# Performance work log

Hardware: AMD Instinct MI355X
Metric: run time of the kernel (lower is better)

Reference implementation:

```python
import jax, jax.numpy as jnp
import numpy as np

DIM = 1024
HEADS = 16
DIM_HEAD = 64
INNER = HEADS * DIM_HEAD
LN_EPS = 1e-5


def setup_inputs() -> dict:
    key = jax.random.key(0)
    ks = jax.random.split(key, 7)
    b, n = 2, 2048
    x = jax.random.normal(ks[0], (b, n, DIM), dtype=jnp.float32)
    attn_bias = jax.random.normal(ks[1], (HEADS, n, n), dtype=jnp.float32)
    gamma = jnp.ones((DIM,), dtype=jnp.float32)
    beta = jnp.zeros((DIM,), dtype=jnp.float32)
    wq = jax.random.normal(ks[2], (DIM, INNER), dtype=jnp.float32) * (DIM ** -0.5)
    wkv = jax.random.normal(ks[3], (DIM, 2 * INNER), dtype=jnp.float32) * (DIM ** -0.5)
    wo = jax.random.normal(ks[4], (INNER, DIM), dtype=jnp.float32) * (INNER ** -0.5)
    return {"x": x, "attn_bias": attn_bias, "gamma": gamma, "beta": beta,
            "wq": wq, "wkv": wkv, "wo": wo}


def reference(x, attn_bias, gamma, beta, wq, wkv, wo):
    b, n, _ = x.shape
    scale = DIM_HEAD ** -0.5
    # LayerNorm
    mu = jnp.mean(x, axis=-1, keepdims=True)
    var = jnp.var(x, axis=-1, keepdims=True)
    xn = (x - mu) * jax.lax.rsqrt(var + LN_EPS) * gamma + beta
    # QKV projections
    q = xn @ wq                      # [b, n, inner]
    kv = xn @ wkv                    # [b, n, 2*inner]
    k, v = jnp.split(kv, 2, axis=-1)
    split_heads = lambda t: t.reshape(b, n, HEADS, DIM_HEAD).transpose(0, 2, 1, 3)
    q, k, v = map(split_heads, (q, k, v))  # [b, h, n, d]
    q = q * scale
    sim = jnp.einsum('bhid,bhjd->bhij', q, k)
    sim = sim + attn_bias[None]      # broadcast over batch
    causal_mask = jnp.triu(jnp.ones((n, n), dtype=bool), k=1)
    sim = jnp.where(causal_mask, -jnp.finfo(sim.dtype).max, sim)
    attn = jax.nn.softmax(sim, axis=-1)
    out = jnp.einsum('bhij,bhjd->bhid', attn, v)
    out = out.transpose(0, 2, 1, 3).reshape(b, n, INNER)
    return out @ wo
```

## Files before the change

### kernel.cpp

```cpp
#include <hip/hip_runtime.h>
#include <hip/hip_bf16.h>

#define DIM   1024
#define HEADS 16
#define DHEAD 64
#define INNER 1024
#define NSEQ  2048
#define NB    2
#define MROWS (NB * NSEQ)
#define QS    (3 * INNER)

typedef __attribute__((ext_vector_type(8))) short    short8;
typedef __attribute__((ext_vector_type(4))) short    short4v;
typedef __attribute__((ext_vector_type(4))) float    floatx4;
typedef __attribute__((ext_vector_type(8))) _Float16 half8;

#define GLOBAL_AS __attribute__((address_space(1)))
#define LDS_AS    __attribute__((address_space(3)))

static __device__ __forceinline__ short f2h(float f) {
  _Float16 h = (_Float16)f;
  return __builtin_bit_cast(short, h);
}
static __device__ __forceinline__ float h2f(short s) {
  return (float)__builtin_bit_cast(_Float16, s);
}

static __device__ __forceinline__ floatx4 mfma16(short8 a, short8 b, floatx4 c) {
  return __builtin_amdgcn_mfma_f32_16x16x32_f16(
      __builtin_bit_cast(half8, a), __builtin_bit_cast(half8, b), c, 0, 0, 0);
}

__device__ __constant__ signed char kQtTab[40] = {
  15,14,13,12,11,10,9,8,7,6,5,4,3,
  15,14,13,12,11,10,9,8,7,
  15,14,13,12,11,
  15,
  2,6,10,14,
  1,5,9,13,
  0,4,8,12};
__device__ __constant__ signed char kCTab[40] = {
  0,0,0,0,0,0,0,0,0,0,0,0,0,
  1,1,1,1,1,1,1,1,1,
  2,2,2,2,2,
  3,
  0,1,2,3,
  0,1,2,3,
  0,1,2,3};
__device__ __constant__ signed char kSlotTab[16][4] = {
  {36,-1,-1,-1},{32,-1,-1,-1},{28,-1,-1,-1},{12,-1,-1,-1},
  {11,37,-1,-1},{10,33,-1,-1},{ 9,29,-1,-1},{ 8,21,-1,-1},
  { 7,20,38,-1},{ 6,19,34,-1},{ 5,18,30,-1},{ 4,17,26,-1},
  { 3,16,25,39},{ 2,15,24,35},{ 1,14,23,31},{ 0,13,22,27}};

__global__ __launch_bounds__(256) void ln_kernel(const float* __restrict__ x,
                                                 const float* __restrict__ gamma,
                                                 const float* __restrict__ beta,
                                                 short* __restrict__ xn) {
  int row = blockIdx.x;
  int t   = threadIdx.x;
  const float4* xr = reinterpret_cast<const float4*>(x + (size_t)row * DIM);
  float4 v = xr[t];
  float s  = v.x + v.y + v.z + v.w;
  float s2 = v.x * v.x + v.y * v.y + v.z * v.z + v.w * v.w;
#pragma unroll
  for (int off = 1; off < 64; off <<= 1) {
    s  += __shfl_xor(s, off);
    s2 += __shfl_xor(s2, off);
  }
  __shared__ float red[8];
  if ((t & 63) == 0) { red[t >> 6] = s; red[(t >> 6) + 4] = s2; }
  __syncthreads();
  s  = red[0] + red[1] + red[2] + red[3];
  s2 = red[4] + red[5] + red[6] + red[7];
  float mu   = s * (1.0f / DIM);
  float var  = s2 * (1.0f / DIM) - mu * mu;
  float rstd = rsqrtf(var + 1e-5f);
  float4 g  = reinterpret_cast<const float4*>(gamma)[t];
  float4 bb = reinterpret_cast<const float4*>(beta)[t];
  short4v o;
  o.x = f2h((v.x - mu) * rstd * g.x + bb.x);
  o.y = f2h((v.y - mu) * rstd * g.y + bb.y);
  o.z = f2h((v.z - mu) * rstd * g.z + bb.z);
  o.w = f2h((v.w - mu) * rstd * g.w + bb.w);
  reinterpret_cast<short4v*>(xn + (size_t)row * DIM)[t] = o;
}

__global__ __launch_bounds__(256) void transpose_f16(const float* __restrict__ w,
                                                     short* __restrict__ wt,
                                                     int Kk, int Nn) {
  __shared__ float tile[32][33];
  int n0 = blockIdx.x * 32, k0 = blockIdx.y * 32;
  int tx = threadIdx.x & 31, ty = threadIdx.x >> 5;
#pragma unroll
  for (int i = 0; i < 32; i += 8)
    tile[ty + i][tx] = w[(size_t)(k0 + ty + i) * Nn + n0 + tx];
  __syncthreads();
#pragma unroll
  for (int i = 0; i < 32; i += 8)
    wt[(size_t)(n0 + ty + i) * Kk + k0 + tx] = f2h(tile[tx][ty + i]);
}

template <bool F32OUT>
__global__ __launch_bounds__(256) void gemm_bt(const short* __restrict__ A,
                                               const short* __restrict__ Bt,
                                               void* __restrict__ Cout,
                                               int Nn, int Kk,
                                               float oscale, float oscale2,
                                               int qsplit) {
  constexpr int BM = 128, BN = 128, BK = 64;
  __shared__ __attribute__((aligned(16))) short As[BM * BK];
  __shared__ __attribute__((aligned(16))) short Bs[BN * BK];
  int bm = blockIdx.x, bn = blockIdx.y;
  int t = threadIdx.x, lane = t & 63, w = t >> 6;
  int l15 = lane & 15, lhi = lane >> 4;
  int wr = w >> 1, wc = w & 1;
  float osc = (bn * BN < qsplit) ? oscale : oscale2;
  floatx4 acc[4][4] = {};
  const short* Ag = A + (size_t)bm * BM * Kk;
  const short* Bg = Bt + (size_t)bn * BN * Kk;

  for (int k0 = 0; k0 < Kk; k0 += BK) {
#pragma unroll
    for (int it = 0; it < 4; ++it) {
      int base = it * 256 + w * 64;
      int idx  = base + lane;
      int row  = idx >> 3, kc = (idx & 7) << 3;
      __builtin_amdgcn_global_load_lds(
          (const GLOBAL_AS unsigned int*)(Ag + (size_t)row * Kk + k0 + kc),
          (LDS_AS unsigned int*)(As + base * 8), 16, 0, 0);
    }
#pragma unroll
    for (int it = 0; it < 4; ++it) {
      int base = it * 256 + w * 64;
      int idx  = base + lane;
      int row  = idx >> 3, kc = (idx & 7) << 3;
      __builtin_amdgcn_global_load_lds(
          (const GLOBAL_AS unsigned int*)(Bg + (size_t)row * Kk + k0 + kc),
          (LDS_AS unsigned int*)(Bs + base * 8), 16, 0, 0);
    }
    __syncthreads();
#pragma unroll
    for (int kc = 0; kc < 2; ++kc) {
      short8 a[4], b[4];
#pragma unroll
      for (int mt = 0; mt < 4; ++mt)
        a[mt] = *reinterpret_cast<const short8*>(
            &As[(wr * 64 + mt * 16 + l15) * BK + lhi * 8 + kc * 32]);
#pragma unroll
      for (int nt = 0; nt < 4; ++nt)
        b[nt] = *reinterpret_cast<const short8*>(
            &Bs[(wc * 64 + nt * 16 + l15) * BK + lhi * 8 + kc * 32]);
#pragma unroll
      for (int mt = 0; mt < 4; ++mt)
#pragma unroll
        for (int nt = 0; nt < 4; ++nt)
          acc[mt][nt] = mfma16(a[mt], b[nt], acc[mt][nt]);
    }
    __syncthreads();
  }

  int row0 = bm * BM + wr * 64;
  int col0 = bn * BN + wc * 64;
#pragma unroll
  for (int mt = 0; mt < 4; ++mt)
#pragma unroll
    for (int nt = 0; nt < 4; ++nt)
#pragma unroll
      for (int r = 0; r < 4; ++r) {
        int row = row0 + mt * 16 + lhi * 4 + r;
        int col = col0 + nt * 16 + l15;
        if (F32OUT)
          ((float*)Cout)[(size_t)row * Nn + col] = acc[mt][nt][r] * osc;
        else
          ((short*)Cout)[(size_t)row * Nn + col] = f2h(acc[mt][nt][r] * osc);
      }
}

__global__ __launch_bounds__(512) void attn_kernel(const short* __restrict__ qkv,
                                                   const float* __restrict__ bias,
                                                   short* __restrict__ ao,
                                                   short* __restrict__ Opart,
                                                   float* __restrict__ mlpart) {
  __shared__ __attribute__((aligned(16))) short Ks[2][2][4096];
  __shared__ __attribute__((aligned(16))) short Vt[2][4096];
  __shared__ __attribute__((aligned(16))) short Ps[128 * 72];

  int p = blockIdx.x;
  int rank = p >> 4, h = p & 15;
  int qt = kQtTab[rank], c = kCTab[rank];
  int tt0 = c * 8;
  int tt1 = 2 * qt + 2; if (tt0 + 8 < tt1) tt1 = tt0 + 8;
  int qb = qt * 128;
  int t = threadIdx.x, lane = t & 63, w = t >> 6;
  int l15 = lane & 15, lhi = lane >> 4;

  short8 qf[2][2];
#pragma unroll
  for (int bb = 0; bb < 2; ++bb) {
    const short* qrow = qkv +
        ((size_t)(bb * NSEQ + qb + w * 16 + l15)) * QS + h * DHEAD + lhi * 8;
    qf[bb][0] = *reinterpret_cast<const short8*>(qrow);
    qf[bb][1] = *reinterpret_cast<const short8*>(qrow + 32);
  }

  int krow = t >> 3;
  int kcg  = (t & 7) ^ (krow & 7);
  int vrr = (t >> 4) * 2, vcc = (t & 15) << 2;
  short4v vr[2][2];

  auto issueK = [&](int tile, int nb) {
#pragma unroll
    for (int bb = 0; bb < 2; ++bb) {
      const short* gp = qkv +
          ((size_t)(bb * NSEQ + tile * 64 + krow)) * QS + INNER + h * DHEAD + kcg * 8;
      __builtin_amdgcn_global_load_lds(
          (const GLOBAL_AS unsigned int*)gp,
          (LDS_AS unsigned int*)(&Ks[nb][bb][0] + (size_t)w * 512), 16, 0, 0);
    }
  };
  auto issueV = [&](int tile) {
#pragma unroll
    for (int bb = 0; bb < 2; ++bb) {
      const short* vp = qkv + ((size_t)(bb * NSEQ + tile * 64 + vrr)) * QS +
                        2 * INNER + h * DHEAD + vcc;
      vr[bb][0] = *reinterpret_cast<const short4v*>(vp);
      vr[bb][1] = *reinterpret_cast<const short4v*>(vp + QS);
    }
  };
  auto writeV = [&]() {
#pragma unroll
    for (int bb = 0; bb < 2; ++bb)
#pragma unroll
      for (int e = 0; e < 4; ++e) {
        int d  = vcc + e;
        int jj = vrr ^ ((d & 7) << 3);
        unsigned int pk = (unsigned short)vr[bb][0][e] |
                          ((unsigned int)(unsigned short)vr[bb][1][e] << 16);
        *reinterpret_cast<unsigned int*>(&Vt[bb][d * 64 + jj]) = pk;
      }
  };
  auto issueB = [&](int tile, floatx4 (&br)[4]) {
    const float* bb0 = bias +
        ((size_t)h * NSEQ + (qb + w * 16 + l15)) * NSEQ + tile * 64 + lhi * 4;
#pragma unroll
    for (int jt = 0; jt < 4; ++jt)
      br[jt] = *reinterpret_cast<const floatx4*>(bb0 + jt * 16);
  };

  float m[2], l[2];
  floatx4 oacc[2][4] = {};
#pragma unroll
  for (int bb = 0; bb < 2; ++bb) { m[bb] = -1e30f; l[bb] = 0.f; }

  int swz = (l15 & 7) << 3;

  auto step = [&](int tt, int KB, floatx4 (&brU)[4], floatx4 (&brN)[4]) {
    bool more = (tt + 1 < tt1);
    if (more) { issueK(tt + 1, KB ^ 1); issueV(tt + 1); issueB(tt + 1, brN); }

#pragma unroll
    for (int bb = 0; bb < 2; ++bb) {
      floatx4 s[4];
#pragma unroll
      for (int jt = 0; jt < 4; ++jt) s[jt] = brU[jt];

#pragma unroll
      for (int jt = 0; jt < 4; ++jt) {
        int ro = (jt * 16 + l15) * 64;
        short8 k0 = *reinterpret_cast<const short8*>(
            &Ks[KB][bb][ro + ((lhi * 8) ^ swz)]);
        short8 k1 = *reinterpret_cast<const short8*>(
            &Ks[KB][bb][ro + ((lhi * 8 + 32) ^ swz)]);
        s[jt] = mfma16(k0, qf[bb][0], s[jt]);
        s[jt] = mfma16(k1, qf[bb][1], s[jt]);
      }

      if (tt >= 2 * qt) {
        int dq = qb + w * 16 + l15 - tt * 64;
#pragma unroll
        for (int jt = 0; jt < 4; ++jt)
#pragma unroll
          for (int r = 0; r < 4; ++r)
            if (jt * 16 + lhi * 4 + r > dq) s[jt][r] = -1e30f;
      }

      float mx = s[0][0];
#pragma unroll
      for (int jt = 0; jt < 4; ++jt)
#pragma unroll
        for (int r = 0; r < 4; ++r) mx = fmaxf(mx, s[jt][r]);
      mx = fmaxf(mx, __shfl_xor(mx, 16));
      mx = fmaxf(mx, __shfl_xor(mx, 32));
      float mnew = fmaxf(m[bb], mx);
      float fac  = __expf(m[bb] - mnew);
      m[bb] = mnew;
      float ps = 0.f;
#pragma unroll
      for (int jt = 0; jt < 4; ++jt)
#pragma unroll
        for (int r = 0; r < 4; ++r) {
          float pv = __expf(s[jt][r] - mnew);
          s[jt][r] = pv;
          ps += pv;
        }
      ps += __shfl_xor(ps, 16);
      ps += __shfl_xor(ps, 32);
      l[bb] = l[bb] * fac + ps;

      float facr[4];
#pragma unroll
      for (int r = 0; r < 4; ++r)
        facr[r] = __shfl(fac, (lane & 48) | (lhi * 4 + r));
#pragma unroll
      for (int dt = 0; dt < 4; ++dt)
#pragma unroll
        for (int r = 0; r < 4; ++r) oacc[bb][dt][r] *= facr[r];

#pragma unroll
      for (int jt = 0; jt < 4; ++jt) {
        short4v pv4;
        pv4.x = f2h(s[jt][0]); pv4.y = f2h(s[jt][1]);
        pv4.z = f2h(s[jt][2]); pv4.w = f2h(s[jt][3]);
        *reinterpret_cast<short4v*>(
            &Ps[(w * 16 + l15) * 72 + jt * 16 + lhi * 4]) = pv4;
      }

#pragma unroll
      for (int jc = 0; jc < 2; ++jc) {
        short8 pf = *reinterpret_cast<const short8*>(
            &Ps[(w * 16 + l15) * 72 + lhi * 8 + jc * 32]);
#pragma unroll
        for (int dt = 0; dt < 4; ++dt) {
          int dd = dt * 16 + l15;
          short8 vf = *reinterpret_cast<const short8*>(
              &Vt[bb][dd * 64 + ((lhi * 8 + jc * 32) ^ swz)]);
          oacc[bb][dt] = mfma16(pf, vf, oacc[bb][dt]);
        }
      }
    }

    if (more) {
      __syncthreads();
      writeV();
      __syncthreads();
    }
  };

  floatx4 brA[4], brB[4];
  issueK(tt0, 0);
  issueV(tt0);
  issueB(tt0, brA);
  __syncthreads();
  writeV();
  __syncthreads();

  int nt = tt1 - tt0;
  for (int i = 0; i < nt; i += 2) {
    step(tt0 + i, 0, brA, brB);
    step(tt0 + i + 1, 1, brB, brA);
  }

  bool single = (tt0 == 0) && (tt1 == 2 * qt + 2);
  if (single) {
#pragma unroll
    for (int bb = 0; bb < 2; ++bb) {
      float linv = 1.f / l[bb];
      float lr[4];
#pragma unroll
      for (int r = 0; r < 4; ++r)
        lr[r] = __shfl(linv, (lane & 48) | (lhi * 4 + r));
#pragma unroll
      for (int dt = 0; dt < 4; ++dt)
#pragma unroll
        for (int r = 0; r < 4; ++r) {
          int row = qb + w * 16 + lhi * 4 + r;
          int col = h * DHEAD + dt * 16 + l15;
          ao[((size_t)(bb * NSEQ + row)) * INNER + col] =
              f2h(oacc[bb][dt][r] * lr[r]);
        }
    }
  } else {
#pragma unroll
    for (int bb = 0; bb < 2; ++bb) {
      size_t pp = ((size_t)h * 40 + rank) * 2 + bb;
      short* Ob = Opart + pp * 8192;
#pragma unroll
      for (int dt = 0; dt < 4; ++dt)
#pragma unroll
        for (int r = 0; r < 4; ++r)
          Ob[(w * 16 + lhi * 4 + r) * 64 + dt * 16 + l15] = f2h(oacc[bb][dt][r]);
      if (lhi == 0) {
        mlpart[pp * 256 + w * 16 + l15] = m[bb];
        mlpart[pp * 256 + 128 + w * 16 + l15] = l[bb];
      }
    }
  }
}

__global__ __launch_bounds__(512) void attn_combine(const short* __restrict__ Opart,
                                                    const float* __restrict__ mlpart,
                                                    short* __restrict__ o) {
  int qt = blockIdx.x + 4, h = blockIdx.y, b = blockIdx.z;
  int nc = (2 * qt + 9) >> 3;
  int t = threadIdx.x, row = t >> 2, cg = (t & 3) << 4;

  float mv[4], lv[4];
  float M = -1e30f;
#pragma unroll
  for (int c2 = 0; c2 < 4; ++c2) {
    if (c2 < nc) {
      size_t pp = ((size_t)h * 40 + kSlotTab[qt][c2]) * 2 + b;
      mv[c2] = mlpart[pp * 256 + row];
      lv[c2] = mlpart[pp * 256 + 128 + row];
      M = fmaxf(M, mv[c2]);
    }
  }

  float acc[16] = {};
  float lsum = 0.f;
#pragma unroll
  for (int c2 = 0; c2 < 4; ++c2) {
    if (c2 >= nc) break;
    float wgt = __expf(mv[c2] - M);
    lsum += wgt * lv[c2];
    size_t pp = ((size_t)h * 40 + kSlotTab[qt][c2]) * 2 + b;
    const short8* Or =
        reinterpret_cast<const short8*>(Opart + pp * 8192 + row * 64 + cg);
    short8 a0 = Or[0], a1 = Or[1];
#pragma unroll
    for (int e = 0; e < 8; ++e) {
      acc[e]     += wgt * h2f(a0[e]);
      acc[8 + e] += wgt * h2f(a1[e]);
    }
  }
  float inv = 1.f / lsum;
  short* op = o + ((size_t)(b * NSEQ + qt * 128 + row)) * INNER + h * DHEAD + cg;
  short8 o0, o1;
#pragma unroll
  for (int e = 0; e < 8; ++e) {
    o0[e] = f2h(acc[e] * inv);
    o1[e] = f2h(acc[8 + e] * inv);
  }
  reinterpret_cast<short8*>(op)[0] = o0;
  reinterpret_cast<short8*>(op)[1] = o1;
}

extern "C" void kernel_launch(void* const* d_in, const int* in_sizes, int n_in,
                              void* d_out, int out_size, void* d_ws, size_t ws_size,
                              hipStream_t stream) {
  const float* x     = (const float*)d_in[0];
  const float* bias  = (const float*)d_in[1];
  const float* gamma = (const float*)d_in[2];
  const float* beta  = (const float*)d_in[3];
  const float* wq    = (const float*)d_in[4];
  const float* wkv   = (const float*)d_in[5];
  const float* wo    = (const float*)d_in[6];
  float* out = (float*)d_out;

  char* ws = (char*)d_ws;
  const size_t MB = 1024 * 1024;
  short* xn      = (short*)(ws);
  short* wqkv_t  = (short*)(ws + 8  * MB);
  short* wo_t    = (short*)(ws + 14 * MB);
  short* qkv     = (short*)(ws + 16 * MB);
  short* Opart   = (short*)(ws + 40 * MB);
  float* mlpart  = (float*)(ws + 62 * MB);
  short* ao      = xn;

  ln_kernel<<<MROWS, 256, 0, stream>>>(x, gamma, beta, xn);
  transpose_f16<<<dim3(INNER / 32, DIM / 32), 256, 0, stream>>>(wq, wqkv_t, DIM, INNER);
  transpose_f16<<<dim3(2 * INNER / 32, DIM / 32), 256, 0, stream>>>(
      wkv, wqkv_t + (size_t)1024 * 1024, DIM, 2 * INNER);
  transpose_f16<<<dim3(DIM / 32, INNER / 32), 256, 0, stream>>>(wo, wo_t, INNER, DIM);

  gemm_bt<false><<<dim3(MROWS / 128, QS / 128), 256, 0, stream>>>(
      xn, wqkv_t, qkv, QS, DIM, 0.125f, 1.0f, 1024);

  attn_kernel<<<640, 512, 0, stream>>>(qkv, bias, ao, Opart, mlpart);
  attn_combine<<<dim3(12, HEADS, NB), 512, 0, stream>>>(Opart, mlpart, ao);

  gemm_bt<true><<<dim3(MROWS / 128, DIM / 128), 256, 0, stream>>>(
      ao, wo_t, out, DIM, INNER, 1.0f, 1.0f, 0);
}
```

Measured before the change: 172.5 us.

## Use 256x256 double-buffered tile for QKV GEMM and XCD-aware block remapping

```diff
diff --git a/kernel.cpp b/kernel.cpp
--- a/kernel.cpp
+++ b/kernel.cpp
@@ -29,6 +29,12 @@
 static __device__ __forceinline__ floatx4 mfma16(short8 a, short8 b, floatx4 c) {
   return __builtin_amdgcn_mfma_f32_16x16x32_f16(
       __builtin_bit_cast(half8, a), __builtin_bit_cast(half8, b), c, 0, 0, 0);
+}
+
+static __device__ __forceinline__ int xcd_work(int bid, int nwg) {
+  int q = nwg >> 3, r = nwg & 7;
+  int xcd = bid & 7, pos = bid >> 3;
+  return (xcd < r ? xcd * (q + 1) : r * (q + 1) + (xcd - r) * q) + pos;
 }
 
 __device__ __constant__ signed char kQtTab[40] = {
@@ -101,21 +107,104 @@
     wt[(size_t)(n0 + ty + i) * Kk + k0 + tx] = f2h(tile[tx][ty + i]);
 }
 
+__global__ __launch_bounds__(512) void gemm_bt256(const short* __restrict__ A,
+                                                  const short* __restrict__ Bt,
+                                                  short* __restrict__ Cout,
+                                                  int Nn, int Kk, int NBN,
+                                                  float oscale, float oscale2,
+                                                  int qsplit) {
+  __shared__ __attribute__((aligned(16))) short As[2][256 * 64];
+  __shared__ __attribute__((aligned(16))) short Bs[2][256 * 64];
+
+  int wk = xcd_work(blockIdx.x, gridDim.x);
+  int bm = wk / NBN, bn = wk % NBN;
+  int t = threadIdx.x, lane = t & 63, w = t >> 6;
+  int l15 = lane & 15, lhi = lane >> 4;
+  int wr = w >> 2, wc = w & 3;
+
+  const short* Ag = A + (size_t)bm * 256 * Kk;
+  const short* Bg = Bt + (size_t)bn * 256 * Kk;
+
+  auto stage = [&](int kt, int buf) {
+#pragma unroll
+    for (int it = 0; it < 4; ++it) {
+      int base = it * 512 + w * 64;
+      int g = base + lane;
+      int row = g >> 3, c8 = (g & 7) << 3;
+      __builtin_amdgcn_global_load_lds(
+          (const GLOBAL_AS unsigned int*)(Ag + (size_t)row * Kk + kt * 64 + c8),
+          (LDS_AS unsigned int*)(&As[buf][base * 8]), 16, 0, 0);
+    }
+#pragma unroll
+    for (int it = 0; it < 4; ++it) {
+      int base = it * 512 + w * 64;
+      int g = base + lane;
+      int row = g >> 3, c8 = (g & 7) << 3;
+      __builtin_amdgcn_global_load_lds(
+          (const GLOBAL_AS unsigned int*)(Bg + (size_t)row * Kk + kt * 64 + c8),
+          (LDS_AS unsigned int*)(&Bs[buf][base * 8]), 16, 0, 0);
+    }
+  };
+
+  floatx4 acc[8][4] = {};
+  int NK = Kk >> 6;
+
+  stage(0, 0);
+  __syncthreads();
+  int cur = 0;
+  for (int kt = 0; kt < NK; ++kt) {
+    if (kt + 1 < NK) stage(kt + 1, cur ^ 1);
+#pragma unroll
+    for (int kc = 0; kc < 2; ++kc) {
+      short8 a[8], b[4];
+#pragma unroll
+      for (int mt = 0; mt < 8; ++mt)
+        a[mt] = *reinterpret_cast<const short8*>(
+            &As[cur][(wr * 128 + mt * 16 + l15) * 64 + kc * 32 + lhi * 8]);
+#pragma unroll
+      for (int nt = 0; nt < 4; ++nt)
+        b[nt] = *reinterpret_cast<const short8*>(
+            &Bs[cur][(wc * 64 + nt * 16 + l15) * 64 + kc * 32 + lhi * 8]);
+#pragma unroll
+      for (int mt = 0; mt < 8; ++mt)
+#pragma unroll
+        for (int nt = 0; nt < 4; ++nt)
+          acc[mt][nt] = mfma16(a[mt], b[nt], acc[mt][nt]);
+    }
+    __syncthreads();
+    cur ^= 1;
+  }
+
+  int row0 = bm * 256 + wr * 128 + lhi * 4;
+  int col0 = bn * 256 + wc * 64 + l15;
+#pragma unroll
+  for (int mt = 0; mt < 8; ++mt)
+#pragma unroll
+    for (int nt = 0; nt < 4; ++nt) {
+      float osc = (bn * 256 + wc * 64 + nt * 16 < qsplit) ? oscale : oscale2;
+#pragma unroll
+      for (int r = 0; r < 4; ++r) {
+        int row = row0 + mt * 16 + r;
+        int col = col0 + nt * 16;
+        Cout[(size_t)row * Nn + col] = f2h(acc[mt][nt][r] * osc);
+      }
+    }
+}
+
 template <bool F32OUT>
 __global__ __launch_bounds__(256) void gemm_bt(const short* __restrict__ A,
                                                const short* __restrict__ Bt,
                                                void* __restrict__ Cout,
-                                               int Nn, int Kk,
-                                               float oscale, float oscale2,
-                                               int qsplit) {
+                                               int Nn, int Kk, int NBN,
+                                               float oscale) {
   constexpr int BM = 128, BN = 128, BK = 64;
   __shared__ __attribute__((aligned(16))) short As[BM * BK];
   __shared__ __attribute__((aligned(16))) short Bs[BN * BK];
-  int bm = blockIdx.x, bn = blockIdx.y;
+  int wk = xcd_work(blockIdx.x, gridDim.x);
+  int bm = wk / NBN, bn = wk % NBN;
   int t = threadIdx.x, lane = t & 63, w = t >> 6;
   int l15 = lane & 15, lhi = lane >> 4;
   int wr = w >> 1, wc = w & 1;
-  float osc = (bn * BN < qsplit) ? oscale : oscale2;
   floatx4 acc[4][4] = {};
   const short* Ag = A + (size_t)bm * BM * Kk;
   const short* Bg = Bt + (size_t)bn * BN * Kk;
@@ -171,9 +260,9 @@
         int row = row0 + mt * 16 + lhi * 4 + r;
         int col = col0 + nt * 16 + l15;
         if (F32OUT)
-          ((float*)Cout)[(size_t)row * Nn + col] = acc[mt][nt][r] * osc;
+          ((float*)Cout)[(size_t)row * Nn + col] = acc[mt][nt][r] * oscale;
         else
-          ((short*)Cout)[(size_t)row * Nn + col] = f2h(acc[mt][nt][r] * osc);
+          ((short*)Cout)[(size_t)row * Nn + col] = f2h(acc[mt][nt][r] * oscale);
       }
 }
 
@@ -474,12 +563,12 @@
       wkv, wqkv_t + (size_t)1024 * 1024, DIM, 2 * INNER);
   transpose_f16<<<dim3(DIM / 32, INNER / 32), 256, 0, stream>>>(wo, wo_t, INNER, DIM);
 
-  gemm_bt<false><<<dim3(MROWS / 128, QS / 128), 256, 0, stream>>>(
-      xn, wqkv_t, qkv, QS, DIM, 0.125f, 1.0f, 1024);
+  gemm_bt256<<<(MROWS / 256) * (QS / 256), 512, 0, stream>>>(
+      xn, wqkv_t, qkv, QS, DIM, QS / 256, 0.125f, 1.0f, 1024);
 
   attn_kernel<<<640, 512, 0, stream>>>(qkv, bias, ao, Opart, mlpart);
   attn_combine<<<dim3(12, HEADS, NB), 512, 0, stream>>>(Opart, mlpart, ao);
 
-  gemm_bt<true><<<dim3(MROWS / 128, DIM / 128), 256, 0, stream>>>(
-      ao, wo_t, out, DIM, INNER, 1.0f, 1.0f, 0);
-}
+  gemm_bt<true><<<(MROWS / 128) * (DIM / 128), 256, 0, stream>>>(
+      ao, wo_t, out, DIM, INNER, DIM / 128, 1.0f);
+}
```

Result: faster. 168.3 us (-2.5%).

## Double-buffer GEMM with swizzled LDS, XCD-aware tile mapping, and fuse prep kernels

Applied to the files above, without the earlier changes.

```diff
diff --git a/kernel.cpp b/kernel.cpp
--- a/kernel.cpp
+++ b/kernel.cpp
@@ -29,6 +29,12 @@
 static __device__ __forceinline__ floatx4 mfma16(short8 a, short8 b, floatx4 c) {
   return __builtin_amdgcn_mfma_f32_16x16x32_f16(
       __builtin_bit_cast(half8, a), __builtin_bit_cast(half8, b), c, 0, 0, 0);
+}
+
+static __device__ __forceinline__ int xcd_work(int bid, int nwg) {
+  int q = nwg >> 3, r = nwg & 7;
+  int xcd = bid & 7, pos = bid >> 3;
+  return (xcd < r ? xcd * (q + 1) : r * (q + 1) + (xcd - r) * q) + pos;
 }
 
 __device__ __constant__ signed char kQtTab[40] = {
@@ -53,119 +59,148 @@
   { 7,20,38,-1},{ 6,19,34,-1},{ 5,18,30,-1},{ 4,17,26,-1},
   { 3,16,25,39},{ 2,15,24,35},{ 1,14,23,31},{ 0,13,22,27}};
 
-__global__ __launch_bounds__(256) void ln_kernel(const float* __restrict__ x,
-                                                 const float* __restrict__ gamma,
-                                                 const float* __restrict__ beta,
-                                                 short* __restrict__ xn) {
-  int row = blockIdx.x;
-  int t   = threadIdx.x;
-  const float4* xr = reinterpret_cast<const float4*>(x + (size_t)row * DIM);
-  float4 v = xr[t];
-  float s  = v.x + v.y + v.z + v.w;
-  float s2 = v.x * v.x + v.y * v.y + v.z * v.z + v.w * v.w;
-#pragma unroll
-  for (int off = 1; off < 64; off <<= 1) {
-    s  += __shfl_xor(s, off);
-    s2 += __shfl_xor(s2, off);
-  }
-  __shared__ float red[8];
-  if ((t & 63) == 0) { red[t >> 6] = s; red[(t >> 6) + 4] = s2; }
+__global__ __launch_bounds__(256) void prep_kernel(
+    const float* __restrict__ x, const float* __restrict__ gamma,
+    const float* __restrict__ beta, short* __restrict__ xn,
+    const float* __restrict__ wq, const float* __restrict__ wkv,
+    const float* __restrict__ wo, short* __restrict__ wqkv_t,
+    short* __restrict__ wo_t) {
+  __shared__ float tile[32][33];
+  int bid = blockIdx.x;
+  int t = threadIdx.x;
+
+  if (bid < MROWS) {
+    const float4* xr = reinterpret_cast<const float4*>(x + (size_t)bid * DIM);
+    float4 v = xr[t];
+    float s  = v.x + v.y + v.z + v.w;
+    float s2 = v.x * v.x + v.y * v.y + v.z * v.z + v.w * v.w;
+#pragma unroll
+    for (int off = 1; off < 64; off <<= 1) {
+      s  += __shfl_xor(s, off);
+      s2 += __shfl_xor(s2, off);
+    }
+    float* red = &tile[0][0];
+    if ((t & 63) == 0) { red[t >> 6] = s; red[(t >> 6) + 4] = s2; }
+    __syncthreads();
+    s  = red[0] + red[1] + red[2] + red[3];
+    s2 = red[4] + red[5] + red[6] + red[7];
+    float mu   = s * (1.0f / DIM);
+    float var  = s2 * (1.0f / DIM) - mu * mu;
+    float rstd = rsqrtf(var + 1e-5f);
+    float4 g  = reinterpret_cast<const float4*>(gamma)[t];
+    float4 bb = reinterpret_cast<const float4*>(beta)[t];
+    short4v o;
+    o.x = f2h((v.x - mu) * rstd * g.x + bb.x);
+    o.y = f2h((v.y - mu) * rstd * g.y + bb.y);
+    o.z = f2h((v.z - mu) * rstd * g.z + bb.z);
+    o.w = f2h((v.w - mu) * rstd * g.w + bb.w);
+    reinterpret_cast<short4v*>(xn + (size_t)bid * DIM)[t] = o;
+    return;
+  }
+
+  bid -= MROWS;
+  const float* src; short* dst; int Nn, nx;
+  if (bid < 1024)      { src = wq;  dst = wqkv_t;                     Nn = 1024; nx = 32; }
+  else if (bid < 3072) { bid -= 1024; src = wkv;
+                         dst = wqkv_t + (size_t)1024 * 1024;          Nn = 2048; nx = 64; }
+  else                 { bid -= 3072; src = wo;  dst = wo_t;          Nn = 1024; nx = 32; }
+  int n0 = (bid % nx) * 32, k0 = (bid / nx) * 32;
+  int tx = t & 31, ty = t >> 5;
+#pragma unroll
+  for (int i = 0; i < 32; i += 8)
+    tile[ty + i][tx] = src[(size_t)(k0 + ty + i) * Nn + n0 + tx];
   __syncthreads();
-  s  = red[0] + red[1] + red[2] + red[3];
-  s2 = red[4] + red[5] + red[6] + red[7];
-  float mu   = s * (1.0f / DIM);
-  float var  = s2 * (1.0f / DIM) - mu * mu;
-  float rstd = rsqrtf(var + 1e-5f);
-  float4 g  = reinterpret_cast<const float4*>(gamma)[t];
-  float4 bb = reinterpret_cast<const float4*>(beta)[t];
-  short4v o;
-  o.x = f2h((v.x - mu) * rstd * g.x + bb.x);
-  o.y = f2h((v.y - mu) * rstd * g.y + bb.y);
-  o.z = f2h((v.z - mu) * rstd * g.z + bb.z);
-  o.w = f2h((v.w - mu) * rstd * g.w + bb.w);
-  reinterpret_cast<short4v*>(xn + (size_t)row * DIM)[t] = o;
-}
-
-__global__ __launch_bounds__(256) void transpose_f16(const float* __restrict__ w,
-                                                     short* __restrict__ wt,
-                                                     int Kk, int Nn) {
-  __shared__ float tile[32][33];
-  int n0 = blockIdx.x * 32, k0 = blockIdx.y * 32;
-  int tx = threadIdx.x & 31, ty = threadIdx.x >> 5;
 #pragma unroll
   for (int i = 0; i < 32; i += 8)
-    tile[ty + i][tx] = w[(size_t)(k0 + ty + i) * Nn + n0 + tx];
-  __syncthreads();
-#pragma unroll
-  for (int i = 0; i < 32; i += 8)
-    wt[(size_t)(n0 + ty + i) * Kk + k0 + tx] = f2h(tile[tx][ty + i]);
+    dst[(size_t)(n0 + ty + i) * 1024 + k0 + tx] = f2h(tile[tx][ty + i]);
 }
 
 template <bool F32OUT>
-__global__ __launch_bounds__(256) void gemm_bt(const short* __restrict__ A,
+__global__ __launch_bounds__(256) void gemm_cv(const short* __restrict__ A,
                                                const short* __restrict__ Bt,
                                                void* __restrict__ Cout,
-                                               int Nn, int Kk,
+                                               int Nn, int Kk, int NBN,
                                                float oscale, float oscale2,
                                                int qsplit) {
-  constexpr int BM = 128, BN = 128, BK = 64;
-  __shared__ __attribute__((aligned(16))) short As[BM * BK];
-  __shared__ __attribute__((aligned(16))) short Bs[BN * BK];
-  int bm = blockIdx.x, bn = blockIdx.y;
+  __shared__ __attribute__((aligned(16))) short As[2][128 * 64];
+  __shared__ __attribute__((aligned(16))) short Bs[2][128 * 64];
+  int wk = xcd_work(blockIdx.x, gridDim.x);
+  int bm = wk / NBN, bn = wk % NBN;
   int t = threadIdx.x, lane = t & 63, w = t >> 6;
   int l15 = lane & 15, lhi = lane >> 4;
   int wr = w >> 1, wc = w & 1;
-  float osc = (bn * BN < qsplit) ? oscale : oscale2;
+  const short* Ag = A + (size_t)bm * 128 * Kk;
+  const short* Bg = Bt + (size_t)bn * 128 * Kk;
+
+  auto stage = [&](int kt, int buf) {
+#pragma unroll
+    for (int it = 0; it < 4; ++it) {
+      int id = it * 256 + t;
+      int row = id >> 3;
+      int cs = ((id & 7) ^ (row & 7)) << 3;
+      __builtin_amdgcn_global_load_lds(
+          (const GLOBAL_AS unsigned int*)(Ag + (size_t)row * Kk + kt * 64 + cs),
+          (LDS_AS unsigned int*)(&As[buf][id * 8]), 16, 0, 0);
+    }
+#pragma unroll
+    for (int it = 0; it < 4; ++it) {
+      int id = it * 256 + t;
+      int row = id >> 3;
+      int cs = ((id & 7) ^ (row & 7)) << 3;
+      __builtin_amdgcn_global_load_lds(
+          (const GLOBAL_AS unsigned int*)(Bg + (size_t)row * Kk + kt * 64 + cs),
+          (LDS_AS unsigned int*)(&Bs[buf][id * 8]), 16, 0, 0);
+    }
+  };
+
   floatx4 acc[4][4] = {};
-  const short* Ag = A + (size_t)bm * BM * Kk;
-  const short* Bg = Bt + (size_t)bn * BN * Kk;
-
-  for (int k0 = 0; k0 < Kk; k0 += BK) {
-#pragma unroll
-    for (int it = 0; it < 4; ++it) {
-      int base = it * 256 + w * 64;
-      int idx  = base + lane;
-      int row  = idx >> 3, kc = (idx & 7) << 3;
-      __builtin_amdgcn_global_load_lds(
-          (const GLOBAL_AS unsigned int*)(Ag + (size_t)row * Kk + k0 + kc),
-          (LDS_AS unsigned int*)(As + base * 8), 16, 0, 0);
-    }
-#pragma unroll
-    for (int it = 0; it < 4; ++it) {
-      int base = it * 256 + w * 64;
-      int idx  = base + lane;
-      int row  = idx >> 3, kc = (idx & 7) << 3;
-      __builtin_amdgcn_global_load_lds(
-          (const GLOBAL_AS unsigned int*)(Bg + (size_t)row * Kk + k0 + kc),
-          (LDS_AS unsigned int*)(Bs + base * 8), 16, 0, 0);
-    }
-    __syncthreads();
+  int NK = Kk >> 6;
+
+  stage(0, 0);
+  stage(1, 1);
+  for (int kt = 0; kt < NK; ++kt) {
+    if (kt + 1 < NK) asm volatile("s_waitcnt vmcnt(8)" ::: "memory");
+    else             asm volatile("s_waitcnt vmcnt(0)" ::: "memory");
+    __builtin_amdgcn_s_barrier();
+    __builtin_amdgcn_sched_barrier(0);
+
+    int buf = kt & 1;
 #pragma unroll
     for (int kc = 0; kc < 2; ++kc) {
       short8 a[4], b[4];
 #pragma unroll
-      for (int mt = 0; mt < 4; ++mt)
-        a[mt] = *reinterpret_cast<const short8*>(
-            &As[(wr * 64 + mt * 16 + l15) * BK + lhi * 8 + kc * 32]);
-#pragma unroll
-      for (int nt = 0; nt < 4; ++nt)
-        b[nt] = *reinterpret_cast<const short8*>(
-            &Bs[(wc * 64 + nt * 16 + l15) * BK + lhi * 8 + kc * 32]);
+      for (int mt = 0; mt < 4; ++mt) {
+        int row = wr * 64 + mt * 16 + l15;
+        int g = (kc * 4 + lhi) ^ (l15 & 7);
+        a[mt] = *reinterpret_cast<const short8*>(&As[buf][row * 64 + g * 8]);
+      }
+#pragma unroll
+      for (int nt = 0; nt < 4; ++nt) {
+        int row = wc * 64 + nt * 16 + l15;
+        int g = (kc * 4 + lhi) ^ (l15 & 7);
+        b[nt] = *reinterpret_cast<const short8*>(&Bs[buf][row * 64 + g * 8]);
+      }
 #pragma unroll
       for (int mt = 0; mt < 4; ++mt)
 #pragma unroll
         for (int nt = 0; nt < 4; ++nt)
           acc[mt][nt] = mfma16(a[mt], b[nt], acc[mt][nt]);
     }
-    __syncthreads();
-  }
-
-  int row0 = bm * BM + wr * 64;
-  int col0 = bn * BN + wc * 64;
+
+    asm volatile("s_waitcnt lgkmcnt(0)" ::: "memory");
+    __builtin_amdgcn_sched_barrier(0);
+    __builtin_amdgcn_s_barrier();
+    __builtin_amdgcn_sched_barrier(0);
+    if (kt + 2 < NK) stage(kt + 2, buf);
+  }
+
+  int row0 = bm * 128 + wr * 64;
+  int col0 = bn * 128 + wc * 64;
 #pragma unroll
   for (int mt = 0; mt < 4; ++mt)
 #pragma unroll
-    for (int nt = 0; nt < 4; ++nt)
+    for (int nt = 0; nt < 4; ++nt) {
+      float osc = (col0 + nt * 16 < qsplit) ? oscale : oscale2;
 #pragma unroll
       for (int r = 0; r < 4; ++r) {
         int row = row0 + mt * 16 + lhi * 4 + r;
@@ -175,6 +210,7 @@
         else
           ((short*)Cout)[(size_t)row * Nn + col] = f2h(acc[mt][nt][r] * osc);
       }
+    }
 }
 
 __global__ __launch_bounds__(512) void attn_kernel(const short* __restrict__ qkv,
@@ -468,18 +504,15 @@
   float* mlpart  = (float*)(ws + 62 * MB);
   short* ao      = xn;
 
-  ln_kernel<<<MROWS, 256, 0, stream>>>(x, gamma, beta, xn);
-  transpose_f16<<<dim3(INNER / 32, DIM / 32), 256, 0, stream>>>(wq, wqkv_t, DIM, INNER);
-  transpose_f16<<<dim3(2 * INNER / 32, DIM / 32), 256, 0, stream>>>(
-      wkv, wqkv_t + (size_t)1024 * 1024, DIM, 2 * INNER);
-  transpose_f16<<<dim3(DIM / 32, INNER / 32), 256, 0, stream>>>(wo, wo_t, INNER, DIM);
-
-  gemm_bt<false><<<dim3(MROWS / 128, QS / 128), 256, 0, stream>>>(
-      xn, wqkv_t, qkv, QS, DIM, 0.125f, 1.0f, 1024);
+  prep_kernel<<<8192, 256, 0, stream>>>(x, gamma, beta, xn, wq, wkv, wo,
+                                        wqkv_t, wo_t);
+
+  gemm_cv<false><<<(MROWS / 128) * (QS / 128), 256, 0, stream>>>(
+      xn, wqkv_t, qkv, QS, DIM, QS / 128, 0.125f, 1.0f, 1024);
 
   attn_kernel<<<640, 512, 0, stream>>>(qkv, bias, ao, Opart, mlpart);
   attn_combine<<<dim3(12, HEADS, NB), 512, 0, stream>>>(Opart, mlpart, ao);
 
-  gemm_bt<true><<<dim3(MROWS / 128, DIM / 128), 256, 0, stream>>>(
-      ao, wo_t, out, DIM, INNER, 1.0f, 1.0f, 0);
-}
+  gemm_cv<true><<<(MROWS / 128) * (DIM / 128), 256, 0, stream>>>(
+      ao, wo_t, out, DIM, INNER, DIM / 128, 1.0f, 1.0f, 0);
+}
```

Result: faster. 151.8 us, median of 2 (-12.0%).
